# Performance work log

Hardware: AMD Instinct MI355X
Metric: run time of the kernel (lower is better)

The kernel has to match this reference:

```python
import jax, jax.numpy as jnp
import numpy as np

HW = [(68, 120), (34, 60), (17, 30)]
STRIDES = [8, 16, 32]
NUM_CLASSES = 11
CENTER_RADIUS = 2.5


def _grids():
    """Flattened per-anchor grid x, grid y and stride, concatenated over levels. [A]"""
    xs, ys, ss = [], [], []
    for (h, w), s in zip(HW, STRIDES):
        yv, xv = jnp.meshgrid(jnp.arange(h, dtype=jnp.float32),
                              jnp.arange(w, dtype=jnp.float32), indexing='ij')
        xs.append(xv.reshape(-1))
        ys.append(yv.reshape(-1))
        ss.append(jnp.full((h * w,), float(s), jnp.float32))
    return jnp.concatenate(xs), jnp.concatenate(ys), jnp.concatenate(ss)


def setup_inputs() -> dict:
    key = jax.random.key(0)
    k1, k2, k3, k4 = jax.random.split(key, 4)
    B, G = 32, 50
    A = sum(h * w for h, w in HW)  # 10710
    preds = jax.random.normal(k1, (B, A, 5 + NUM_CLASSES), jnp.float32)
    cls = jax.random.randint(k2, (B, G, 1), 0, NUM_CLASSES).astype(jnp.float32)
    cxcy = jax.random.uniform(k3, (B, G, 2), jnp.float32) * jnp.array([960.0, 544.0], jnp.float32)
    wh = 10.0 + 90.0 * jax.random.uniform(k4, (B, G, 2), jnp.float32)
    labels = jnp.concatenate([cls, cxcy, wh], -1)
    valid = (jnp.arange(G) < 40)[None, :, None].astype(jnp.float32)  # last 10 rows are padding (num_gt=40)
    labels = labels * valid
    return {"preds": preds, "labels": labels}


def _decode(preds):
    # YOLOX get_output_and_grid: xy = (pred_xy + grid) * stride; wh = exp(pred_wh) * stride
    xg, yg, s = _grids()
    xy = (preds[..., :2] + jnp.stack([xg, yg], -1)) * s[:, None]
    wh = jnp.exp(preds[..., 2:4]) * s[:, None]
    return jnp.concatenate([xy, wh, preds[..., 4:]], -1)


def _in_boxes_info(labels, valid):
    # labels: [B, G, 5] (cls, cx, cy, w, h); valid: [B, G] bool
    xg, yg, s = _grids()
    xc = (xg + 0.5) * s  # anchor center x, [A]
    yc = (yg + 0.5) * s  # anchor center y, [A]
    gx, gy = labels[..., 1, None], labels[..., 2, None]  # [B, G, 1]
    gw, gh = labels[..., 3, None], labels[..., 4, None]
    xcb = xc[None, None, :]  # [1, 1, A]
    ycb = yc[None, None, :]
    # inside gt box: all four signed distances > 0
    in_box = (jnp.minimum(jnp.minimum(xcb - (gx - 0.5 * gw), (gx + 0.5 * gw) - xcb),
                          jnp.minimum(ycb - (gy - 0.5 * gh), (gy + 0.5 * gh) - ycb)) > 0.0)
    # inside center region of radius 2.5*stride
    r = CENTER_RADIUS * s[None, None, :]
    in_ctr = (jnp.minimum(jnp.minimum(xcb - (gx - r), (gx + r) - xcb),
                          jnp.minimum(ycb - (gy - r), (gy + r) - ycb)) > 0.0)
    v = valid[:, :, None]
    in_box = in_box & v
    in_ctr = in_ctr & v
    fg_mask = jnp.any(in_box | in_ctr, axis=1)  # [B, A] : is_in_boxes_anchor
    in_box_and_ctr = in_box & in_ctr & fg_mask[:, None, :]  # [B, G, A]
    return fg_mask, in_box_and_ctr


def reference(preds, labels):
    # Decode raw head outputs to image-space boxes (batched over all levels)
    decoded = _decode(preds)  # [B, A, 16]
    # Per-image SimOTA in-box / in-center candidate masks.
    # Original slices columns by fg_mask (dynamic shape); we return the full
    # [B, G, A] mask zeroed outside fg columns / invalid gts -- same information.
    valid = jnp.sum(labels, axis=2) > 0  # [B, G], mirrors n_label logic
    fg_mask, in_box_and_ctr = _in_boxes_info(labels, valid)
    return decoded, fg_mask, in_box_and_ctr
```

## Files before the change

kernel.cpp:

```cpp
#include <hip/hip_runtime.h>
#include <math.h>

#define BATCH 32
#define NGT   50
#define ATOT  10710
#define NCH   16
#define L0_END 8160
#define L1_END 10200

__global__ __launch_bounds__(256) void simota_fused_kernel(
    const float* __restrict__ preds,
    const float* __restrict__ labels,
    float* __restrict__ out_decoded,
    float* __restrict__ out_fg,
    float* __restrict__ out_ibc)
{
    const int b   = blockIdx.y;
    const int a   = blockIdx.x * blockDim.x + threadIdx.x;
    const int tid = threadIdx.x;

    __shared__ float s_gx[NGT], s_gy[NGT];
    __shared__ float s_xlo[NGT], s_xhi[NGT], s_ylo[NGT], s_yhi[NGT];
    __shared__ int   s_valid[NGT];
    if (tid < NGT) {
        const float* lr = labels + ((size_t)b * NGT + tid) * 5;
        float l0 = lr[0], gx = lr[1], gy = lr[2], gw = lr[3], gh = lr[4];
        float sum = l0 + gx + gy + gw + gh;
        s_valid[tid] = (sum > 0.0f) ? 1 : 0;
        float hw = 0.5f * gw;
        float hh = 0.5f * gh;
        s_gx[tid]  = gx;        s_gy[tid]  = gy;
        s_xlo[tid] = gx - hw;   s_xhi[tid] = gx + hw;
        s_ylo[tid] = gy - hh;   s_yhi[tid] = gy + hh;
    }
    __syncthreads();
    if (a >= ATOT) return;

    int w, la; float s;
    if (a < L0_END)      { w = 120; s = 8.0f;  la = a; }
    else if (a < L1_END) { w = 60;  s = 16.0f; la = a - L0_END; }
    else                 { w = 30;  s = 32.0f; la = a - L1_END; }
    const float xg = (float)(la % w);
    const float yg = (float)(la / w);

    const float* p = preds + ((size_t)b * ATOT + a) * NCH;
    float4 p0 = ((const float4*)p)[0];
    float4 p1 = ((const float4*)p)[1];
    float4 p2 = ((const float4*)p)[2];
    float4 p3 = ((const float4*)p)[3];
    float4 d0;
    d0.x = (p0.x + xg) * s;
    d0.y = (p0.y + yg) * s;
    d0.z = expf(p0.z) * s;
    d0.w = expf(p0.w) * s;
    float* dptr = out_decoded + ((size_t)b * ATOT + a) * NCH;
    ((float4*)dptr)[0] = d0;
    ((float4*)dptr)[1] = p1;
    ((float4*)dptr)[2] = p2;
    ((float4*)dptr)[3] = p3;

    const float xc = (xg + 0.5f) * s;
    const float yc = (yg + 0.5f) * s;
    const float r  = 2.5f * s;

    int fg = 0;
    float* ibc = out_ibc + (size_t)b * NGT * ATOT + a;
    #pragma unroll 10
    for (int g = 0; g < NGT; ++g) {
        const int   v  = s_valid[g];
        const float gx = s_gx[g], gy = s_gy[g];
        float bx = fminf(xc - s_xlo[g], s_xhi[g] - xc);
        float by = fminf(yc - s_ylo[g], s_yhi[g] - yc);
        int in_box = ((fminf(bx, by) > 0.0f) ? 1 : 0) & v;
        float cx = fminf(xc - (gx - r), (gx + r) - xc);
        float cy = fminf(yc - (gy - r), (gy + r) - yc);
        int in_ctr = ((fminf(cx, cy) > 0.0f) ? 1 : 0) & v;
        fg |= (in_box | in_ctr);
        ibc[(size_t)g * ATOT] = (in_box & in_ctr) ? 1.0f : 0.0f;
    }
    out_fg[(size_t)b * ATOT + a] = fg ? 1.0f : 0.0f;
}

extern "C" void kernel_launch(void* const* d_in, const int* in_sizes, int n_in,
                              void* d_out, int out_size, void* d_ws, size_t ws_size,
                              hipStream_t stream) {
    const float* preds  = (const float*)d_in[0];
    const float* labels = (const float*)d_in[1];
    float* out = (float*)d_out;
    float* out_decoded = out;
    float* out_fg      = out + (size_t)BATCH * ATOT * NCH;
    float* out_ibc     = out + (size_t)BATCH * ATOT * NCH + (size_t)BATCH * ATOT;

    dim3 grid((ATOT + 255) / 256, BATCH);
    dim3 block(256);
    simota_fused_kernel<<<grid, block, 0, stream>>>(preds, labels, out_decoded, out_fg, out_ibc);
}
```

Before: 119.1 us.

## Process two anchors per thread with nontemporal vector stores and 64-thread blocks

Each thread now handles an adjacent pair of anchors (level widths are even, so pairs never straddle rows or levels). This allows 8-byte stores for the mask outputs and 128-byte contiguous loads and stores of preds. All global traffic uses nontemporal loads and stores, gt parameters are packed into float4 shared arrays, and blocks shrink to 64 threads. The aim is fewer, wider memory transactions on this write-bound kernel. The trade-off is more work per thread and smaller blocks that each redo the label setup.

```diff
diff --git a/kernel.cpp b/kernel.cpp
--- a/kernel.cpp
+++ b/kernel.cpp
@@ -7,8 +7,12 @@
 #define NCH   16
 #define L0_END 8160
 #define L1_END 10200
+#define APAIR 5355
 
-__global__ __launch_bounds__(256) void simota_fused_kernel(
+typedef float f32x4 __attribute__((ext_vector_type(4)));
+typedef float f32x2 __attribute__((ext_vector_type(2)));
+
+__global__ __launch_bounds__(64) void simota_fused_kernel(
     const float* __restrict__ preds,
     const float* __restrict__ labels,
     float* __restrict__ out_decoded,
@@ -16,69 +20,80 @@
     float* __restrict__ out_ibc)
 {
     const int b   = blockIdx.y;
-    const int a   = blockIdx.x * blockDim.x + threadIdx.x;
     const int tid = threadIdx.x;
+    const int pi  = blockIdx.x * 64 + tid;
 
-    __shared__ float s_gx[NGT], s_gy[NGT];
-    __shared__ float s_xlo[NGT], s_xhi[NGT], s_ylo[NGT], s_yhi[NGT];
-    __shared__ int   s_valid[NGT];
+    __shared__ f32x4 s_box[NGT];
+    __shared__ f32x4 s_ctr[NGT];
     if (tid < NGT) {
         const float* lr = labels + ((size_t)b * NGT + tid) * 5;
         float l0 = lr[0], gx = lr[1], gy = lr[2], gw = lr[3], gh = lr[4];
         float sum = l0 + gx + gy + gw + gh;
-        s_valid[tid] = (sum > 0.0f) ? 1 : 0;
-        float hw = 0.5f * gw;
-        float hh = 0.5f * gh;
-        s_gx[tid]  = gx;        s_gy[tid]  = gy;
-        s_xlo[tid] = gx - hw;   s_xhi[tid] = gx + hw;
-        s_ylo[tid] = gy - hh;   s_yhi[tid] = gy + hh;
+        float vf  = (sum > 0.0f) ? 1.0f : 0.0f;
+        float hw = 0.5f * gw, hh = 0.5f * gh;
+        s_box[tid] = (f32x4){gx - hw, gx + hw, gy - hh, gy + hh};
+        s_ctr[tid] = (f32x4){gx, gy, vf, 0.0f};
     }
     __syncthreads();
-    if (a >= ATOT) return;
+    if (pi >= APAIR) return;
 
+    const int a0 = 2 * pi;
     int w, la; float s;
-    if (a < L0_END)      { w = 120; s = 8.0f;  la = a; }
-    else if (a < L1_END) { w = 60;  s = 16.0f; la = a - L0_END; }
-    else                 { w = 30;  s = 32.0f; la = a - L1_END; }
-    const float xg = (float)(la % w);
-    const float yg = (float)(la / w);
+    if (a0 < L0_END)      { w = 120; s = 8.0f;  la = a0; }
+    else if (a0 < L1_END) { w = 60;  s = 16.0f; la = a0 - L0_END; }
+    else                  { w = 30;  s = 32.0f; la = a0 - L1_END; }
+    const float xg0 = (float)(la % w);
+    const float xg1 = xg0 + 1.0f;
+    const float yg  = (float)(la / w);
 
-    const float* p = preds + ((size_t)b * ATOT + a) * NCH;
-    float4 p0 = ((const float4*)p)[0];
-    float4 p1 = ((const float4*)p)[1];
-    float4 p2 = ((const float4*)p)[2];
-    float4 p3 = ((const float4*)p)[3];
-    float4 d0;
-    d0.x = (p0.x + xg) * s;
-    d0.y = (p0.y + yg) * s;
-    d0.z = expf(p0.z) * s;
-    d0.w = expf(p0.w) * s;
-    float* dptr = out_decoded + ((size_t)b * ATOT + a) * NCH;
-    ((float4*)dptr)[0] = d0;
-    ((float4*)dptr)[1] = p1;
-    ((float4*)dptr)[2] = p2;
-    ((float4*)dptr)[3] = p3;
+    const float* p = preds + ((size_t)b * ATOT + a0) * NCH;
+    f32x4 q[8];
+    #pragma unroll
+    for (int i = 0; i < 8; ++i)
+        q[i] = __builtin_nontemporal_load(((const f32x4*)p) + i);
+    q[0].x = (q[0].x + xg0) * s;
+    q[0].y = (q[0].y + yg ) * s;
+    q[0].z = expf(q[0].z) * s;
+    q[0].w = expf(q[0].w) * s;
+    q[4].x = (q[4].x + xg1) * s;
+    q[4].y = (q[4].y + yg ) * s;
+    q[4].z = expf(q[4].z) * s;
+    q[4].w = expf(q[4].w) * s;
+    f32x4* dptr = (f32x4*)(out_decoded + ((size_t)b * ATOT + a0) * NCH);
+    #pragma unroll
+    for (int i = 0; i < 8; ++i)
+        __builtin_nontemporal_store(q[i], dptr + i);
 
-    const float xc = (xg + 0.5f) * s;
-    const float yc = (yg + 0.5f) * s;
-    const float r  = 2.5f * s;
+    const float xc0 = (xg0 + 0.5f) * s;
+    const float xc1 = (xg1 + 0.5f) * s;
+    const float yc  = (yg  + 0.5f) * s;
+    const float r   = 2.5f * s;
 
-    int fg = 0;
-    float* ibc = out_ibc + (size_t)b * NGT * ATOT + a;
-    #pragma unroll 10
+    float fg0 = 0.0f, fg1 = 0.0f;
+    float* ibc = out_ibc + (size_t)b * NGT * ATOT + a0;
+    #pragma unroll 5
     for (int g = 0; g < NGT; ++g) {
-        const int   v  = s_valid[g];
-        const float gx = s_gx[g], gy = s_gy[g];
-        float bx = fminf(xc - s_xlo[g], s_xhi[g] - xc);
-        float by = fminf(yc - s_ylo[g], s_yhi[g] - yc);
-        int in_box = ((fminf(bx, by) > 0.0f) ? 1 : 0) & v;
-        float cx = fminf(xc - (gx - r), (gx + r) - xc);
-        float cy = fminf(yc - (gy - r), (gy + r) - yc);
-        int in_ctr = ((fminf(cx, cy) > 0.0f) ? 1 : 0) & v;
-        fg |= (in_box | in_ctr);
-        ibc[(size_t)g * ATOT] = (in_box & in_ctr) ? 1.0f : 0.0f;
+        const f32x4 bx = s_box[g];
+        const f32x4 cg = s_ctr[g];
+        float by = fminf(yc - bx.z, bx.w - yc);
+        float b0 = fminf(fminf(xc0 - bx.x, bx.y - xc0), by);
+        float b1 = fminf(fminf(xc1 - bx.x, bx.y - xc1), by);
+        float txl = cg.x - r, txh = cg.x + r;
+        float tyl = cg.y - r, tyh = cg.y + r;
+        float cy = fminf(yc - tyl, tyh - yc);
+        float c0 = fminf(fminf(xc0 - txl, txh - xc0), cy);
+        float c1 = fminf(fminf(xc1 - txl, txh - xc1), cy);
+        const float vf = cg.z;
+        float o0 = (fminf(b0, c0) > 0.0f) ? vf : 0.0f;
+        float o1 = (fminf(b1, c1) > 0.0f) ? vf : 0.0f;
+        fg0 = fmaxf(fg0, vf * fmaxf(b0, c0));
+        fg1 = fmaxf(fg1, vf * fmaxf(b1, c1));
+        __builtin_nontemporal_store((f32x2){o0, o1},
+                                    (f32x2*)(ibc + (size_t)g * ATOT));
     }
-    out_fg[(size_t)b * ATOT + a] = fg ? 1.0f : 0.0f;
+    __builtin_nontemporal_store(
+        (f32x2){fg0 > 0.0f ? 1.0f : 0.0f, fg1 > 0.0f ? 1.0f : 0.0f},
+        (f32x2*)(out_fg + (size_t)b * ATOT + a0));
 }
 
 extern "C" void kernel_launch(void* const* d_in, const int* in_sizes, int n_in,
@@ -91,7 +106,7 @@
     float* out_fg      = out + (size_t)BATCH * ATOT * NCH;
     float* out_ibc     = out + (size_t)BATCH * ATOT * NCH + (size_t)BATCH * ATOT;
 
-    dim3 grid((ATOT + 255) / 256, BATCH);
-    dim3 block(256);
+    dim3 grid((APAIR + 63) / 64, BATCH);
+    dim3 block(64);
     simota_fused_kernel<<<grid, block, 0, stream>>>(preds, labels, out_decoded, out_fg, out_ibc);
 }
```

After: 161.0 us. +35.1%, slower.
